# Kernel optimization log

Measured on AMD Instinct MI355X. Metric: run time of the kernel, lower is better.

Reference implementation:

```python
import jax, jax.numpy as jnp
import numpy as np


def setup_inputs() -> dict:
    key = jax.random.key(0)
    kq, kk, kv = jax.random.split(key, 3)
    B, H, S, D = 4, 16, 2048, 64
    q = jax.random.normal(kq, (B, H, S, D), dtype=jnp.float32)
    k = jax.random.normal(kk, (B, H, S, D), dtype=jnp.float32)
    v = jax.random.normal(kv, (B, H, S, D), dtype=jnp.float32)
    # BERT-style additive mask (0 = attend, large negative = masked); all-attend here.
    attention_mask = jnp.zeros((B, 1, 1, S), dtype=jnp.float32)
    return {"q": q, "k": k, "v": v, "attention_mask": attention_mask,
            "attention_head_size": D}


def reference(q, k, v, attention_mask, attention_head_size):
    # scores: [B,H,S,S] = Q K^T / sqrt(d)
    scale = 1.0 / jnp.sqrt(jnp.asarray(attention_head_size, dtype=q.dtype))
    scores = jnp.einsum("bhqd,bhkd->bhqk", q, k) * scale
    scores = scores + attention_mask  # additive mask broadcast over [B,1,1,S]
    probs = jax.nn.softmax(scores, axis=-1)
    # dropout is identity in eval mode (original code's dropout call is broken anyway)
    out = jnp.einsum("bhqk,bhkd->bhqd", probs, v)
    return out
```

## Files before the change

### kernel.cpp

```cpp
#include <hip/hip_runtime.h>


typedef __attribute__((ext_vector_type(8))) short short8;
typedef __attribute__((ext_vector_type(4))) float floatx4;

#define S_LEN 2048
#define D_DIM 64
#define NT    32
#define L2E   1.44269504089f
#define MFIX  12.0f

static __device__ __forceinline__ unsigned short f2b(float x) {
  union { float f; unsigned int u; } c; c.f = x;
  return (unsigned short)((c.u + 0x7FFFu + ((c.u >> 16) & 1u)) >> 16);
}
static __device__ __forceinline__ unsigned int rhu(float x) {
  union { float f; unsigned int u; } c; c.f = x;
  return (c.u + 0x8000u) >> 16;
}
static __device__ __forceinline__ void load_lds16(const void* g, void* l) {
  __builtin_amdgcn_global_load_lds(
      (const __attribute__((address_space(1))) unsigned int*)g,
      (__attribute__((address_space(3))) unsigned int*)l, 16, 0, 0);
}

__global__ __launch_bounds__(256) void prep_kernel(
    const float* __restrict__ kin, const float* __restrict__ vin,
    unsigned short* __restrict__ kb, unsigned short* __restrict__ vt) {
  const int tid = threadIdx.x, bx = blockIdx.x;
  if (bx < 1024) {
    const int bh = bx >> 4;
    const int k0 = (bx & 15) * 128;
    const int kg = tid & 15;
    const int dg = tid >> 4;
    const float* vp = vin + ((size_t)bh * S_LEN + k0 + kg * 8) * D_DIM + dg * 4;
    float4 f[8];
#pragma unroll
    for (int j = 0; j < 8; ++j) f[j] = *(const float4*)(vp + j * D_DIM);
    const float* ff = (const float*)&f[0];
    const int t  = (k0 >> 6) + (kg >> 3);
    const int ww = (kg >> 1) & 3;
    const int c0 = (kg & 1) * 2;
    const int s  = dg & 3;
    unsigned short* vbase = vt + (((size_t)bh * 32 + t) * 4 + ww) * 1024;
#pragma unroll
    for (int i = 0; i < 4; ++i) {
      const int r = dg * 4 + i;
      uint2 a, bb;
      a.x  = (unsigned)f2b(ff[0 * 4 + i]) | ((unsigned)f2b(ff[1 * 4 + i]) << 16);
      a.y  = (unsigned)f2b(ff[2 * 4 + i]) | ((unsigned)f2b(ff[3 * 4 + i]) << 16);
      bb.x = (unsigned)f2b(ff[4 * 4 + i]) | ((unsigned)f2b(ff[5 * 4 + i]) << 16);
      bb.y = (unsigned)f2b(ff[6 * 4 + i]) | ((unsigned)f2b(ff[7 * 4 + i]) << 16);
      uint4 o;
      if (s & 1) { o.x = bb.x; o.y = bb.y; o.z = a.x;  o.w = a.y;  }
      else       { o.x = a.x;  o.y = a.y;  o.z = bb.x; o.w = bb.y; }
      *(uint4*)(vbase + r * 16 + ((c0 ^ (s & 2)) * 4)) = o;
    }
  } else {
    const int i = ((bx - 1024) * 256 + tid) * 8;
    const float4 f0 = *(const float4*)(kin + i);
    const float4 f1 = *(const float4*)(kin + i + 4);
    uint4 o;
    o.x = (unsigned)f2b(f0.x) | ((unsigned)f2b(f0.y) << 16);
    o.y = (unsigned)f2b(f0.z) | ((unsigned)f2b(f0.w) << 16);
    o.z = (unsigned)f2b(f1.x) | ((unsigned)f2b(f1.y) << 16);
    o.w = (unsigned)f2b(f1.z) | ((unsigned)f2b(f1.w) << 16);
    *(uint4*)(kb + i) = o;
  }
}

union SMem {
  struct {
    unsigned short K[2][64 * 64];
    unsigned short V[4][2][64 * 16];
  } m;
  float Os[64][68];
};

__global__ __launch_bounds__(256, 3) void flash_kernel(
    const float* __restrict__ qin, const unsigned short* __restrict__ kb,
    const unsigned short* __restrict__ vt, const float* __restrict__ mask,
    float* __restrict__ out) {
  __shared__ SMem sm;
  __shared__ float Ls[4][64];

  const int tid = threadIdx.x;
  const int w = tid >> 6, lane = tid & 63, quad = lane >> 4, lm = lane & 15;
  const int bx = blockIdx.x, bh = blockIdx.y, b = bh >> 4;
  const int q0 = bx * 64;
  const int l7 = lm & 7;

  unsigned short* Qs = sm.m.K[1];
  {
    const int row = tid >> 2, r7 = row & 7;
    const float* qp = qin + ((size_t)(bh * S_LEN + q0 + row)) * D_DIM + (tid & 3) * 16;
#pragma unroll
    for (int h = 0; h < 2; ++h) {
      const int chunk = (tid & 3) * 2 + h;
      float4 a = *(const float4*)(qp + h * 8);
      float4 c = *(const float4*)(qp + h * 8 + 4);
      uint4 o;
      o.x = (unsigned)f2b(a.x * 0.125f) | ((unsigned)f2b(a.y * 0.125f) << 16);
      o.y = (unsigned)f2b(a.z * 0.125f) | ((unsigned)f2b(a.w * 0.125f) << 16);
      o.z = (unsigned)f2b(c.x * 0.125f) | ((unsigned)f2b(c.y * 0.125f) << 16);
      o.w = (unsigned)f2b(c.z * 0.125f) | ((unsigned)f2b(c.w * 0.125f) << 16);
      *(uint4*)&Qs[row * 64 + ((chunk ^ r7) * 8)] = o;
    }
  }

  const int rl = lane >> 3, cl = lane & 7;
  const int swz = (cl ^ rl) * 8;
  const unsigned short* kp0 = kb + (size_t)bh * S_LEN * D_DIM + (w * 16 + rl) * 64 + swz;
  const unsigned short* kp1 = kp0 + 8 * 64;
  const unsigned short* vsrcV = vt + (size_t)bh * (NT * 4096) + w * 1024 + lane * 8;
  const int ldsA = (w * 16) * 64, ldsB = (w * 16 + 8) * 64;

  load_lds16(kp0, &sm.m.K[0][ldsA]);
  load_lds16(kp1, &sm.m.K[0][ldsB]);
  load_lds16(vsrcV, &sm.m.V[w][0][0]);
  load_lds16(vsrcV + 512, &sm.m.V[w][0][512]);

  const float* mrow = mask + b * S_LEN + w * 16 + quad * 4;
  floatx4 mc;
  {
    const floatx4 ml = *(const floatx4*)mrow;
#pragma unroll
    for (int r = 0; r < 4; ++r) mc[r] = fmaf(ml[r], L2E, -MFIX * L2E);
  }

  __syncthreads();

  short8 bq[4][2];
#pragma unroll
  for (int qs = 0; qs < 4; ++qs) {
    bq[qs][0] = *(const short8*)&Qs[(qs * 16 + lm) * 64 + ((quad ^ l7) * 8)];
    bq[qs][1] = *(const short8*)&Qs[(qs * 16 + lm) * 64 + (((4 + quad) ^ l7) * 8)];
  }
  __syncthreads();

  const int kidx0 = (w * 16 + lm) * 64 + ((quad ^ l7) * 8);
  const int kidx1 = (w * 16 + lm) * 64 + (((4 + quad) ^ l7) * 8);
  const int vidx = lm * 16 + ((quad ^ ((lm >> 2) & 3)) * 4);

  const short8 ones = (short8){0x3F80, 0x3F80, 0x3F80, 0x3F80,
                               0x3F80, 0x3F80, 0x3F80, 0x3F80};

  floatx4 o[4][4];
#pragma unroll
  for (int dt = 0; dt < 4; ++dt)
#pragma unroll
    for (int qs = 0; qs < 4; ++qs) o[dt][qs] = (floatx4){0.f, 0.f, 0.f, 0.f};
  floatx4 lacc[4];
#pragma unroll
  for (int qs = 0; qs < 4; ++qs) lacc[qs] = (floatx4){0.f, 0.f, 0.f, 0.f};
  uint4 pb[4];
  uint2 vcarry[4];

#pragma unroll 2
  for (int t = 0; t < NT; ++t) {
    const unsigned short* kcur = (t & 1) ? sm.m.K[1] : sm.m.K[0];
    const unsigned short* vcur = &sm.m.V[w][t & 1][0];
    floatx4 mnext;
    if (t + 1 < NT) {
      unsigned short* knext = (t & 1) ? sm.m.K[0] : sm.m.K[1];
      unsigned short* vnext = &sm.m.V[w][(t + 1) & 1][0];
      const size_t off = (size_t)(t + 1) * 4096;
      load_lds16(kp0 + off, knext + ldsA);
      load_lds16(kp1 + off, knext + ldsB);
      load_lds16(vsrcV + (t + 1) * 4096, vnext);
      load_lds16(vsrcV + (t + 1) * 4096 + 512, vnext + 512);
      mnext = *(const floatx4*)(mrow + (t + 1) * 64);
      asm volatile("s_waitcnt vmcnt(5)" ::: "memory");
    } else {
      asm volatile("s_waitcnt vmcnt(0)" ::: "memory");
    }
    __builtin_amdgcn_sched_barrier(0);

    const short8 ak0 = *(const short8*)&kcur[kidx0];
    const short8 ak1 = *(const short8*)&kcur[kidx1];

    if ((t & 1) == 0) {
#pragma unroll
      for (int dt = 0; dt < 4; ++dt)
        vcarry[dt] = *(const uint2*)&vcur[dt * 256 + vidx];
    }

#pragma unroll
    for (int qs = 0; qs < 4; ++qs) {
      floatx4 st = (floatx4){0.f, 0.f, 0.f, 0.f};
      st = __builtin_amdgcn_mfma_f32_16x16x32_bf16(ak0, bq[qs][0], st, 0, 0, 0);
      st = __builtin_amdgcn_mfma_f32_16x16x32_bf16(ak1, bq[qs][1], st, 0, 0, 0);
      float p[4];
#pragma unroll
      for (int r = 0; r < 4; ++r)
        p[r] = __builtin_amdgcn_exp2f(fmaf(st[r], L2E, mc[r]));
      const unsigned lo = rhu(p[0]) | (rhu(p[1]) << 16);
      const unsigned hi = rhu(p[2]) | (rhu(p[3]) << 16);
      if ((t & 1) == 0) { pb[qs].x = lo; pb[qs].y = hi; }
      else             { pb[qs].z = lo; pb[qs].w = hi; }
    }

    if (t & 1) {
#pragma unroll
      for (int dt = 0; dt < 4; ++dt) {
        union { uint2 u2[2]; short8 s; } av;
        av.u2[0] = vcarry[dt];
        av.u2[1] = *(const uint2*)&vcur[dt * 256 + vidx];
#pragma unroll
        for (int qs = 0; qs < 4; ++qs) {
          union { uint4 u; short8 s; } bp;
          bp.u = pb[qs];
          o[dt][qs] = __builtin_amdgcn_mfma_f32_16x16x32_bf16(av.s, bp.s, o[dt][qs], 0, 0, 0);
        }
      }
#pragma unroll
      for (int qs = 0; qs < 4; ++qs) {
        union { uint4 u; short8 s; } bp;
        bp.u = pb[qs];
        lacc[qs] = __builtin_amdgcn_mfma_f32_16x16x32_bf16(ones, bp.s, lacc[qs], 0, 0, 0);
      }
    }

    if (t + 1 < NT) {
#pragma unroll
      for (int r = 0; r < 4; ++r) mc[r] = fmaf(mnext[r], L2E, -MFIX * L2E);
    }
  }

  if (quad == 0) {
#pragma unroll
    for (int qs = 0; qs < 4; ++qs) Ls[w][qs * 16 + lm] = lacc[qs][0];
  }

#pragma unroll
  for (int ph = 0; ph < 4; ++ph) {
    __syncthreads();
    if (w == ph) {
#pragma unroll
      for (int dt = 0; dt < 4; ++dt)
#pragma unroll
        for (int qs = 0; qs < 4; ++qs) {
          float* dst = &sm.Os[qs * 16 + lm][dt * 16 + quad * 4];
          if (ph == 0) {
            *(floatx4*)dst = o[dt][qs];
          } else {
            floatx4 cur = *(const floatx4*)dst;
            *(floatx4*)dst = cur + o[dt][qs];
          }
        }
    }
  }
  __syncthreads();

  {
    const int q = tid >> 2, dc = (tid & 3) * 16;
    const float l = Ls[0][q] + Ls[1][q] + Ls[2][q] + Ls[3][q];
    const float inv = 1.0f / l;
    float* outp = out + ((size_t)(bh * S_LEN + q0 + q)) * D_DIM + dc;
#pragma unroll
    for (int i = 0; i < 4; ++i) {
      floatx4 v = *(const floatx4*)&sm.Os[q][dc + i * 4];
      v *= inv;
      *(floatx4*)(outp + i * 4) = v;
    }
  }
}

extern "C" void kernel_launch(void* const* d_in, const int* in_sizes, int n_in,
                              void* d_out, int out_size, void* d_ws, size_t ws_size,
                              hipStream_t stream) {
  const float* q = (const float*)d_in[0];
  const float* k = (const float*)d_in[1];
  const float* v = (const float*)d_in[2];
  const float* mask = (const float*)d_in[3];
  float* out = (float*)d_out;

  unsigned short* kb = (unsigned short*)d_ws;
  unsigned short* vt = kb + (size_t)64 * S_LEN * D_DIM;

  prep_kernel<<<1024 + 4096, 256, 0, stream>>>(k, v, kb, vt);
  flash_kernel<<<dim3(32, 64), 256, 0, stream>>>(q, kb, vt, mask, out);
}
```

Before: 264.5 us.

## Stage V transpose through LDS for coalesced stores; sum softmax denominator with VALU

The V preprocessing kernel now builds the transposed bf16 tile in a swizzled shared-memory buffer and then writes it out in contiguous 16-byte chunks, instead of scattering stores straight to global memory. In the attention kernel, the row-sum of probabilities is no longer computed with an extra MFMA against a ones vector. Each lane now accumulates the fp32 exp values itself and the partial sums are reduced with cross-lane shuffles at the end. This removes four MFMAs per iteration pair but adds VALU adds in the inner loop. The sum is now taken over unrounded fp32 values rather than the bf16-rounded ones fed to the PV matmul, which slightly changes the normalisation.

New measurement: 227.9 us. 1.16x faster.

```diff
diff --git a/kernel.cpp b/kernel.cpp
--- a/kernel.cpp
+++ b/kernel.cpp
@@ -29,20 +29,22 @@
     unsigned short* __restrict__ kb, unsigned short* __restrict__ vt) {
   const int tid = threadIdx.x, bx = blockIdx.x;
   if (bx < 1024) {
+    __shared__ unsigned short M[8 * 1024];
     const int bh = bx >> 4;
     const int k0 = (bx & 15) * 128;
-    const int kg = tid & 15;
-    const int dg = tid >> 4;
+    const int t0 = (bx & 15) * 2;
+    const int kg = tid >> 4;
+    const int dg = tid & 15;
     const float* vp = vin + ((size_t)bh * S_LEN + k0 + kg * 8) * D_DIM + dg * 4;
     float4 f[8];
 #pragma unroll
     for (int j = 0; j < 8; ++j) f[j] = *(const float4*)(vp + j * D_DIM);
     const float* ff = (const float*)&f[0];
-    const int t  = (k0 >> 6) + (kg >> 3);
+    const int t_loc = kg >> 3;
     const int ww = (kg >> 1) & 3;
     const int c0 = (kg & 1) * 2;
     const int s  = dg & 3;
-    unsigned short* vbase = vt + (((size_t)bh * 32 + t) * 4 + ww) * 1024;
+    const int blk = t_loc * 4 + ww;
 #pragma unroll
     for (int i = 0; i < 4; ++i) {
       const int r = dg * 4 + i;
@@ -54,7 +56,20 @@
       uint4 o;
       if (s & 1) { o.x = bb.x; o.y = bb.y; o.z = a.x;  o.w = a.y;  }
       else       { o.x = a.x;  o.y = a.y;  o.z = bb.x; o.w = bb.y; }
-      *(uint4*)(vbase + r * 16 + ((c0 ^ (s & 2)) * 4)) = o;
+      const int H = (c0 ^ (s & 2)) >> 1;
+      const int m = r * 2 + H;
+      const int mp = m ^ ((r >> 2) & 7);
+      *(uint4*)&M[blk * 1024 + mp * 8] = o;
+    }
+    __syncthreads();
+    unsigned short* dstb = vt + ((size_t)bh * 32 + t0) * 4096;
+    const int cblk = tid >> 5;
+#pragma unroll
+    for (int rd = 0; rd < 4; ++rd) {
+      const int j = (tid & 31) + rd * 32;
+      const int jp = j ^ ((j >> 3) & 7);
+      const uint4 v = *(const uint4*)&M[cblk * 1024 + jp * 8];
+      *(uint4*)(dstb + cblk * 1024 + j * 8) = v;
     }
   } else {
     const int i = ((bx - 1024) * 256 + tid) * 8;
@@ -142,17 +157,12 @@
   const int kidx1 = (w * 16 + lm) * 64 + (((4 + quad) ^ l7) * 8);
   const int vidx = lm * 16 + ((quad ^ ((lm >> 2) & 3)) * 4);
 
-  const short8 ones = (short8){0x3F80, 0x3F80, 0x3F80, 0x3F80,
-                               0x3F80, 0x3F80, 0x3F80, 0x3F80};
-
   floatx4 o[4][4];
 #pragma unroll
   for (int dt = 0; dt < 4; ++dt)
 #pragma unroll
     for (int qs = 0; qs < 4; ++qs) o[dt][qs] = (floatx4){0.f, 0.f, 0.f, 0.f};
-  floatx4 lacc[4];
-#pragma unroll
-  for (int qs = 0; qs < 4; ++qs) lacc[qs] = (floatx4){0.f, 0.f, 0.f, 0.f};
+  float lsum[4] = {0.f, 0.f, 0.f, 0.f};
   uint4 pb[4];
   uint2 vcarry[4];
 
@@ -192,8 +202,10 @@
       st = __builtin_amdgcn_mfma_f32_16x16x32_bf16(ak1, bq[qs][1], st, 0, 0, 0);
       float p[4];
 #pragma unroll
-      for (int r = 0; r < 4; ++r)
+      for (int r = 0; r < 4; ++r) {
         p[r] = __builtin_amdgcn_exp2f(fmaf(st[r], L2E, mc[r]));
+        lsum[qs] += p[r];
+      }
       const unsigned lo = rhu(p[0]) | (rhu(p[1]) << 16);
       const unsigned hi = rhu(p[2]) | (rhu(p[3]) << 16);
       if ((t & 1) == 0) { pb[qs].x = lo; pb[qs].y = hi; }
@@ -213,12 +225,6 @@
           o[dt][qs] = __builtin_amdgcn_mfma_f32_16x16x32_bf16(av.s, bp.s, o[dt][qs], 0, 0, 0);
         }
       }
-#pragma unroll
-      for (int qs = 0; qs < 4; ++qs) {
-        union { uint4 u; short8 s; } bp;
-        bp.u = pb[qs];
-        lacc[qs] = __builtin_amdgcn_mfma_f32_16x16x32_bf16(ones, bp.s, lacc[qs], 0, 0, 0);
-      }
     }
 
     if (t + 1 < NT) {
@@ -227,9 +233,16 @@
     }
   }
 
+#pragma unroll
+  for (int qs = 0; qs < 4; ++qs) {
+    float v = lsum[qs];
+    v += __shfl_xor(v, 16, 64);
+    v += __shfl_xor(v, 32, 64);
+    lsum[qs] = v;
+  }
   if (quad == 0) {
 #pragma unroll
-    for (int qs = 0; qs < 4; ++qs) Ls[w][qs * 16 + lm] = lacc[qs][0];
+    for (int qs = 0; qs < 4; ++qs) Ls[w][qs * 16 + lm] = lsum[qs];
   }
 
 #pragma unroll
```
